# Kernel optimization log

Hardware: AMD Instinct MI355X
Metric: run time of the kernel (lower is better)

## Reference

```python
import jax, jax.numpy as jnp
import numpy as np

B, S, HID = 2, 2048, 4096
H, KV, D = 32, 8, 128
WINDOW = 512
ROPE_THETA = 10000.0


def _rope(x, positions):
    # x: [B, S, h, D]; neox rotate-half over full head_dim
    half = D // 2
    inv_freq = 1.0 / (ROPE_THETA ** (jnp.arange(0, half, dtype=jnp.float32) / half))
    ang = positions.astype(jnp.float32)[..., None] * inv_freq  # [B,S,half]
    cos = jnp.cos(ang)[:, :, None, :]
    sin = jnp.sin(ang)[:, :, None, :]
    x1, x2 = x[..., :half], x[..., half:]
    return jnp.concatenate([x1 * cos - x2 * sin, x2 * cos + x1 * sin], axis=-1)


def _smooth(x, filt):
    # x: [B, S, KV, D]; filt: [2, KV] -> out[t] = prev[t-1]*filt[0] + cur[t]*filt[1]
    prev = jnp.pad(x[:, :-1], ((0, 0), (1, 0), (0, 0), (0, 0)))  # zero at t=0
    return x * filt[1][None, None, :, None] + prev * filt[0][None, None, :, None]


def setup_inputs() -> dict:
    key = jax.random.key(0)
    k1, k2, k3, k4, k5 = jax.random.split(key, 5)
    return {
        "hidden_states": jax.random.normal(k1, (B, S, HID), jnp.float32) * 0.02,
        "positions": jnp.broadcast_to(jnp.arange(S, dtype=jnp.int32), (B, S)),
        "w_pack": jax.random.normal(k2, (HID, (H + 2 * KV) * D), jnp.float32) * (HID ** -0.5),
        "w_o": jax.random.normal(k3, (H * D, HID), jnp.float32) * ((H * D) ** -0.5),
        "conv_k": jax.random.normal(k4, (2, KV), jnp.float32) * 0.5,
        "conv_v": jax.random.normal(k5, (2, KV), jnp.float32) * 0.5,
    }


def reference(hidden_states, positions, w_pack, w_o, conv_k, conv_v):
    qkv = jnp.einsum("bsh,hf->bsf", hidden_states, w_pack)
    q = qkv[..., : H * D].reshape(B, S, H, D)
    k = qkv[..., H * D : (H + KV) * D].reshape(B, S, KV, D)
    v = qkv[..., (H + KV) * D :].reshape(B, S, KV, D)

    # causal depthwise smoothing of k/v (window 2), BEFORE rope
    k = _smooth(k, conv_k)
    v = _smooth(v, conv_v)

    q = _rope(q, positions)
    k = _rope(k, positions)

    g = H // KV  # GQA group size
    k_rep = jnp.repeat(k, g, axis=2)  # [B,S,H,D]
    v_rep = jnp.repeat(v, g, axis=2)

    scale = D ** -0.5
    scores = jnp.einsum("bqhd,bkhd->bhqk", q, k_rep) * scale
    qi = jnp.arange(S)[:, None]
    ki = jnp.arange(S)[None, :]
    mask = (ki <= qi) & (qi - ki < WINDOW)  # causal sliding window
    scores = jnp.where(mask[None, None], scores, jnp.float32(-1e30))
    probs = jax.nn.softmax(scores, axis=-1)
    attn = jnp.einsum("bhqk,bkhd->bqhd", probs, v_rep).reshape(B, S, H * D)
    return jnp.einsum("bsf,fh->bsh", attn, w_o)
```

## Files before the change

kernel.cpp:

```cpp
#include <hip/hip_runtime.h>
#include <stdint.h>

typedef unsigned short u16;
typedef unsigned int   u32;
typedef __bf16 bf16_t;
typedef __attribute__((ext_vector_type(8))) bf16_t bf16x8;
typedef __attribute__((ext_vector_type(4))) float   f32x4;

#define AS_GLOBAL __attribute__((address_space(1)))
#define AS_LDS    __attribute__((address_space(3)))

__device__ __forceinline__ void glds16(const u16* g, u16* l) {
  __builtin_amdgcn_global_load_lds((const AS_GLOBAL u32*)g, (AS_LDS u32*)l, 16, 0, 0);
}
__device__ __forceinline__ u16 f2bf(float f) {
  union { float f; u32 u; } a; a.f = f;
  return (u16)((a.u + 0x7FFFu + ((a.u >> 16) & 1u)) >> 16);
}
__device__ __forceinline__ float bf2f(u16 s) {
  union { u32 u; float f; } a; a.u = ((u32)s) << 16;
  return a.f;
}
union U16x8 { uint4 u; bf16x8 v; };

__global__ __launch_bounds__(256) void cvt_bf16(const float* __restrict__ X, u16* __restrict__ Y) {
  int i = blockIdx.x * 256 + threadIdx.x;
  float4 v = ((const float4*)X)[i];
  ushort4 o; o.x = f2bf(v.x); o.y = f2bf(v.y); o.z = f2bf(v.z); o.w = f2bf(v.w);
  ((ushort4*)Y)[i] = o;
}

__global__ __launch_bounds__(256) void cvt_transpose(const float* __restrict__ W, u16* __restrict__ Wt,
                                                     int K, int N) {
  __shared__ float t[64][65];
  const int n0 = blockIdx.x * 64, k0 = blockIdx.y * 64;
  const int tid = threadIdx.x;
  const int cr = tid >> 4, cc = (tid & 15) * 4;
#pragma unroll
  for (int p = 0; p < 4; ++p) {
    int r = p * 16 + cr;
    float4 v = *(const float4*)&W[(size_t)(k0 + r) * N + n0 + cc];
    t[r][cc] = v.x; t[r][cc + 1] = v.y; t[r][cc + 2] = v.z; t[r][cc + 3] = v.w;
  }
  __syncthreads();
#pragma unroll
  for (int p = 0; p < 4; ++p) {
    int rr = p * 16 + cr;
    ushort4 o;
    o.x = f2bf(t[cc + 0][rr]); o.y = f2bf(t[cc + 1][rr]);
    o.z = f2bf(t[cc + 2][rr]); o.w = f2bf(t[cc + 3][rr]);
    *(ushort4*)&Wt[(size_t)(n0 + rr) * K + k0 + cc] = o;
  }
}

template <int WRITE_BF16>
__global__ __launch_bounds__(256) void gemm_bt(const u16* __restrict__ A, const u16* __restrict__ Bt,
                                               void* __restrict__ C, int N, int K) {
  __shared__ u16 lA[128 * 32];
  __shared__ u16 lB[128 * 32];
  const int tid = threadIdx.x;
  const int w = tid >> 6, l = tid & 63;
  const int col = l & 15, quad = l >> 4;
  const int m0 = blockIdx.y * 128, n0 = blockIdx.x * 128;
  const int wm = (w >> 1) * 64, wn = (w & 1) * 64;

  f32x4 acc[4][4];
#pragma unroll
  for (int i = 0; i < 4; ++i)
#pragma unroll
    for (int j = 0; j < 4; ++j) acc[i][j] = f32x4{0.f, 0.f, 0.f, 0.f};

  const int srow = l >> 2, scol = (l & 3) * 8;
  const u16* Ab = A + (size_t)m0 * K;
  const u16* Bb = Bt + (size_t)n0 * K;

  for (int k0 = 0; k0 < K; k0 += 32) {
    __syncthreads();
#pragma unroll
    for (int i = 0; i < 2; ++i) {
      int chunk = w * 2 + i;
      int row = chunk * 16 + srow;
      glds16(Ab + (size_t)row * K + k0 + scol, &lA[chunk * 512]);
      glds16(Bb + (size_t)row * K + k0 + scol, &lB[chunk * 512]);
    }
    __syncthreads();
    bf16x8 af[4], bfr[4];
#pragma unroll
    for (int t = 0; t < 4; ++t) {
      af[t]  = *(const bf16x8*)&lA[(wm + t * 16 + col) * 32 + quad * 8];
      bfr[t] = *(const bf16x8*)&lB[(wn + t * 16 + col) * 32 + quad * 8];
    }
#pragma unroll
    for (int i = 0; i < 4; ++i)
#pragma unroll
      for (int j = 0; j < 4; ++j)
        acc[i][j] = __builtin_amdgcn_mfma_f32_16x16x32_bf16(af[i], bfr[j], acc[i][j], 0, 0, 0);
  }
  if (WRITE_BF16) {
    u16* Cb = (u16*)C;
#pragma unroll
    for (int i = 0; i < 4; ++i)
#pragma unroll
      for (int r = 0; r < 4; ++r) {
        int m = m0 + wm + i * 16 + quad * 4 + r;
        u16* rp = Cb + (size_t)m * N + n0 + wn + col;
#pragma unroll
        for (int j = 0; j < 4; ++j) rp[j * 16] = f2bf(acc[i][j][r]);
      }
  } else {
    float* Cf = (float*)C;
#pragma unroll
    for (int i = 0; i < 4; ++i)
#pragma unroll
      for (int r = 0; r < 4; ++r) {
        int m = m0 + wm + i * 16 + quad * 4 + r;
        float* rp = Cf + (size_t)m * N + n0 + wn + col;
#pragma unroll
        for (int j = 0; j < 4; ++j) rp[j * 16] = acc[i][j][r];
      }
  }
}

__global__ __launch_bounds__(256) void smooth_rope(const u16* __restrict__ QKV, const int* __restrict__ pos,
                                                   const float* __restrict__ ck, const float* __restrict__ cv,
                                                   u16* __restrict__ Q, u16* __restrict__ Kk, u16* __restrict__ V) {
  const int s = blockIdx.x, b = blockIdx.y, tid = threadIdx.x;
  const size_t base = (size_t)(b * 2048 + s) * 6144;
  const bool hasPrev = (s > 0);
  const size_t prev = base - 6144;
  const float p = (float)pos[b * 2048 + s];
  const float L2F = 0.20762050593046f;

  for (int e = tid; e < 2048; e += 256) {
    int h = e >> 6, i = e & 63;
    float x1 = bf2f(QKV[base + h * 128 + i]);
    float x2 = bf2f(QKV[base + h * 128 + 64 + i]);
    float ang = p * exp2f(-(float)i * L2F);
    float sn, cs; __sincosf(ang, &sn, &cs);
    size_t o = ((size_t)(b * 32 + h) * 2048 + s) * 128 + i;
    Q[o] = f2bf(x1 * cs - x2 * sn);
    Q[o + 64] = f2bf(x2 * cs + x1 * sn);
  }
  for (int e = tid; e < 512; e += 256) {
    int kv = e >> 6, i = e & 63;
    size_t off = 4096 + (size_t)kv * 128;
    float f0 = ck[kv], f1 = ck[8 + kv];
    float x1 = bf2f(QKV[base + off + i]) * f1;
    float x2 = bf2f(QKV[base + off + 64 + i]) * f1;
    if (hasPrev) {
      x1 += bf2f(QKV[prev + off + i]) * f0;
      x2 += bf2f(QKV[prev + off + 64 + i]) * f0;
    }
    float ang = p * exp2f(-(float)i * L2F);
    float sn, cs; __sincosf(ang, &sn, &cs);
    size_t o = ((size_t)(b * 8 + kv) * 2048 + s) * 128 + i;
    Kk[o] = f2bf(x1 * cs - x2 * sn);
    Kk[o + 64] = f2bf(x2 * cs + x1 * sn);
  }
  for (int e = tid; e < 1024; e += 256) {
    int kv = e >> 7, d = e & 127;
    size_t off = 5120 + (size_t)kv * 128 + d;
    float f0 = cv[kv], f1 = cv[8 + kv];
    float x = bf2f(QKV[base + off]) * f1;
    if (hasPrev) x += bf2f(QKV[prev + off]) * f0;
    V[((size_t)(b * 8 + kv) * 2048 + s) * 128 + d] = f2bf(x);
  }
}

__global__ __launch_bounds__(256) void transpose_v(const u16* __restrict__ V, u16* __restrict__ Vt) {
  __shared__ u16 t[64][72];
  const int s0 = blockIdx.x * 64, d0 = blockIdx.y * 64, bkv = blockIdx.z;
  const u16* src = V + (size_t)bkv * 2048 * 128;
  u16* dst = Vt + (size_t)bkv * 128 * 2048;
  const int tid = threadIdx.x;
  for (int e = tid; e < 4096; e += 256) {
    int r = e >> 6, c = e & 63;
    t[r][c] = src[(size_t)(s0 + r) * 128 + d0 + c];
  }
  __syncthreads();
  for (int e = tid; e < 4096; e += 256) {
    int r = e >> 6, c = e & 63;
    dst[(size_t)(d0 + r) * 2048 + s0 + c] = t[c][r];
  }
}

__global__ __launch_bounds__(256) void attn_fwd(const u16* __restrict__ Q, const u16* __restrict__ Kk,
                                                const u16* __restrict__ Vt, u16* __restrict__ O) {
  __shared__ union {
    struct { u16 k[64 * 136]; u16 v[128 * 72]; u16 p[4][16 * 72]; } s;
    u16 epi[64 * 136];
  } sm;
  const int tid = threadIdx.x, w = tid >> 6, l = tid & 63;
  const int col = l & 15, quad = l >> 4;
  const int q0 = blockIdx.x * 64;
  const int bh = blockIdx.y;
  const int b = bh >> 5, h = bh & 31, kv = h >> 2;
  const int qrow = q0 + w * 16 + col;
  const int qlo = q0 + w * 16;

  bf16x8 qf[4];
  {
    const u16* qp = Q + ((size_t)((b * 32 + h) * 2048 + qrow)) * 128 + quad * 8;
#pragma unroll
    for (int dc = 0; dc < 4; ++dc) { U16x8 u; u.u = *(const uint4*)(qp + dc * 32); qf[dc] = u.v; }
  }
  const u16* Kbase = Kk + (size_t)(b * 8 + kv) * 2048 * 128;
  const u16* Vbase = Vt + (size_t)(b * 8 + kv) * 128 * 2048;

  f32x4 of[8];
#pragma unroll
  for (int i = 0; i < 8; ++i) of[i] = f32x4{0.f, 0.f, 0.f, 0.f};
  float m_i = -3.0e38f, l_i = 0.f;

  const int s_lo = q0 >= 511 ? q0 - 511 : 0;
  const int kt_lo = s_lo >> 6, kt_hi = q0 >> 6;

  for (int kt = kt_lo; kt <= kt_hi; ++kt) {
    const int k0 = kt * 64;
    __syncthreads();
    for (int sg = tid; sg < 1024; sg += 256) {
      int kr = sg >> 4, kc = sg & 15;
      uint4 kd = *(const uint4*)(Kbase + (size_t)(k0 + kr) * 128 + kc * 8);
      *(uint4*)&sm.s.k[kr * 136 + kc * 8] = kd;
      int vr = sg >> 3, vc = sg & 7;
      uint4 vd = *(const uint4*)(Vbase + (size_t)vr * 2048 + k0 + vc * 8);
      *(uint4*)&sm.s.v[vr * 72 + vc * 8] = vd;
    }
    __syncthreads();

    f32x4 st[4];
#pragma unroll
    for (int t = 0; t < 4; ++t) {
      st[t] = f32x4{0.f, 0.f, 0.f, 0.f};
#pragma unroll
      for (int dc = 0; dc < 4; ++dc) {
        bf16x8 a = *(const bf16x8*)&sm.s.k[(t * 16 + col) * 136 + dc * 32 + quad * 8];
        st[t] = __builtin_amdgcn_mfma_f32_16x16x32_bf16(a, qf[dc], st[t], 0, 0, 0);
      }
    }
    const bool full = (k0 + 63 <= qlo) && (qlo + 15 - k0 < 512);
    float pmax = -3.0e38f;
#pragma unroll
    for (int t = 0; t < 4; ++t)
#pragma unroll
      for (int r = 0; r < 4; ++r) {
        float v = st[t][r] * 0.08838834764831845f;
        if (!full) {
          int key = k0 + t * 16 + quad * 4 + r;
          if (key > qrow || qrow - key >= 512) v = -1.0e30f;
        }
        st[t][r] = v;
        pmax = fmaxf(pmax, v);
      }
    pmax = fmaxf(pmax, __shfl_xor(pmax, 16, 64));
    pmax = fmaxf(pmax, __shfl_xor(pmax, 32, 64));
    float m_new = fmaxf(m_i, pmax);
    float alpha = __expf(m_i - m_new);
    float rsum = 0.f;
#pragma unroll
    for (int t = 0; t < 4; ++t) {
      u16 pk[4];
#pragma unroll
      for (int r = 0; r < 4; ++r) {
        float e = __expf(st[t][r] - m_new);
        rsum += e;
        pk[r] = f2bf(e);
      }
      u32 lo = (u32)pk[0] | ((u32)pk[1] << 16);
      u32 hi = (u32)pk[2] | ((u32)pk[3] << 16);
      *(uint2*)&sm.s.p[w][col * 72 + t * 16 + quad * 4] = make_uint2(lo, hi);
    }
    rsum += __shfl_xor(rsum, 16, 64);
    rsum += __shfl_xor(rsum, 32, 64);
    l_i = l_i * alpha + rsum;
    m_i = m_new;
#pragma unroll
    for (int i = 0; i < 8; ++i) {
      of[i][0] *= alpha; of[i][1] *= alpha; of[i][2] *= alpha; of[i][3] *= alpha;
    }
#pragma unroll
    for (int c = 0; c < 2; ++c) {
      bf16x8 pb = *(const bf16x8*)&sm.s.p[w][col * 72 + c * 32 + quad * 8];
#pragma unroll
      for (int dt = 0; dt < 8; ++dt) {
        bf16x8 a = *(const bf16x8*)&sm.s.v[(dt * 16 + col) * 72 + c * 32 + quad * 8];
        of[dt] = __builtin_amdgcn_mfma_f32_16x16x32_bf16(a, pb, of[dt], 0, 0, 0);
      }
    }
  }
  float invl = 1.f / l_i;
  __syncthreads();
#pragma unroll
  for (int dt = 0; dt < 8; ++dt) {
    u16 pk[4];
#pragma unroll
    for (int r = 0; r < 4; ++r) pk[r] = f2bf(of[dt][r] * invl);
    u32 lo = (u32)pk[0] | ((u32)pk[1] << 16);
    u32 hi = (u32)pk[2] | ((u32)pk[3] << 16);
    *(uint2*)&sm.epi[(w * 16 + col) * 136 + dt * 16 + quad * 4] = make_uint2(lo, hi);
  }
  __syncthreads();
  for (int e = tid; e < 1024; e += 256) {
    int r = e >> 4, c = e & 15;
    uint4 v = *(const uint4*)&sm.epi[r * 136 + c * 8];
    *(uint4*)(O + ((size_t)(b * 2048 + q0 + r) * 4096 + h * 128 + c * 8)) = v;
  }
}

extern "C" void kernel_launch(void* const* d_in, const int* in_sizes, int n_in,
                              void* d_out, int out_size, void* d_ws, size_t ws_size,
                              hipStream_t stream) {
  const float* hs  = (const float*)d_in[0];
  const int*   pos = (const int*)d_in[1];
  const float* wp  = (const float*)d_in[2];
  const float* wo  = (const float*)d_in[3];
  const float* ck  = (const float*)d_in[4];
  const float* cv  = (const float*)d_in[5];
  float* out = (float*)d_out;
  char* ws = (char*)d_ws;

  u16* Xb   = (u16*)(ws);
  u16* Wt   = (u16*)(ws + 33554432);
  u16* QKV  = (u16*)(ws + 83886080);
  u16* Qb   = (u16*)(ws + 134217728);
  u16* Kb   = (u16*)(ws + 167772160);
  u16* Vb   = (u16*)(ws + 176160768);
  u16* Vtb  = (u16*)(ws + 184549376);
  u16* Attn = Xb;
  u16* Wot  = Wt;

  cvt_bf16<<<16384, 256, 0, stream>>>(hs, Xb);
  cvt_transpose<<<dim3(96, 64), 256, 0, stream>>>(wp, Wt, 4096, 6144);
  gemm_bt<1><<<dim3(48, 32), 256, 0, stream>>>(Xb, Wt, (void*)QKV, 6144, 4096);
  smooth_rope<<<dim3(2048, 2), 256, 0, stream>>>(QKV, pos, ck, cv, Qb, Kb, Vb);
  transpose_v<<<dim3(32, 2, 16), 256, 0, stream>>>(Vb, Vtb);
  attn_fwd<<<dim3(32, 64), 256, 0, stream>>>(Qb, Kb, Vtb, Attn);
  cvt_transpose<<<dim3(64, 64), 256, 0, stream>>>(wo, Wot, 4096, 4096);
  gemm_bt<0><<<dim3(32, 32), 256, 0, stream>>>(Attn, Wot, (void*)out, 4096, 4096);
}
```

Baseline: 808.8 us.

## Replace GEMM with 512-thread double-buffered swizzled 256xBN tile kernel

Replaces the simple 128x128 single-buffered GEMM with a 512-thread kernel that computes 256xBN tiles (BN=192 for QKV, 256 for the output projection). It double-buffers LDS with a K-step of 64 and issues the next stage's global-to-LDS loads in between the MFMA phases, using explicit vmcnt waits and raw barriers. LDS rows use an XOR swizzle to avoid bank conflicts, and s_setprio raises priority around the MFMA bursts. The aim is to hide memory latency and raise MFMA utilisation in the two big GEMMs. In exchange the kernel uses many more registers and more LDS per block, and the hand-tuned waitcnt counts are fragile.

```diff
diff --git a/kernel.cpp b/kernel.cpp
--- a/kernel.cpp
+++ b/kernel.cpp
@@ -53,70 +53,148 @@
   }
 }
 
-template <int WRITE_BF16>
-__global__ __launch_bounds__(256) void gemm_bt(const u16* __restrict__ A, const u16* __restrict__ Bt,
-                                               void* __restrict__ C, int N, int K) {
-  __shared__ u16 lA[128 * 32];
-  __shared__ u16 lB[128 * 32];
+__device__ __forceinline__ void stage256(const u16* gb, u16* ldst, int K, int kc, int tid, int w) {
+#pragma unroll
+  for (int s = 0; s < 2; ++s) {
+    int t = s * 512 + tid;
+    int row = t >> 2;
+    int slot = (t & 3) ^ ((row >> 1) & 3);
+    glds16(gb + (size_t)row * K + kc + slot * 8, ldst + s * 4096 + w * 512);
+  }
+}
+template <int BN>
+__device__ __forceinline__ void stageB(const u16* gb, u16* ldst, int K, int k0, int tid, int w) {
+  constexpr int NB = BN / 64;
+#pragma unroll
+  for (int s = 0; s < NB; ++s) {
+    int t = s * 512 + tid;
+    int rr = t >> 2;
+    int kh = rr >= BN ? 1 : 0;
+    int row = rr - kh * BN;
+    int slot = (t & 3) ^ ((row >> 1) & 3);
+    glds16(gb + (size_t)row * K + k0 + kh * 32 + slot * 8, ldst + s * 4096 + w * 512);
+  }
+}
+
+template <int BN, int WRITE_BF16>
+__global__ __launch_bounds__(512, 2) void gemm8p(const u16* __restrict__ A, const u16* __restrict__ Bt,
+                                                 void* __restrict__ C, int N, int K) {
+  constexpr int NF = BN / 64;
+  constexpr int NB = BN / 64;
+  constexpr int A_U16 = 2 * 256 * 32;
+  constexpr int B_U16 = 2 * BN * 32;
+  constexpr int BUF = A_U16 + B_U16;
+  __shared__ __align__(16) u16 lds[2 * BUF];
+
   const int tid = threadIdx.x;
   const int w = tid >> 6, l = tid & 63;
   const int col = l & 15, quad = l >> 4;
-  const int m0 = blockIdx.y * 128, n0 = blockIdx.x * 128;
-  const int wm = (w >> 1) * 64, wn = (w & 1) * 64;
-
-  f32x4 acc[4][4];
-#pragma unroll
-  for (int i = 0; i < 4; ++i)
-#pragma unroll
-    for (int j = 0; j < 4; ++j) acc[i][j] = f32x4{0.f, 0.f, 0.f, 0.f};
-
-  const int srow = l >> 2, scol = (l & 3) * 8;
+  const int m0 = blockIdx.y * 256, n0 = blockIdx.x * BN;
+  const int wm = (w >> 2) * 128;
+  const int wn = (w & 3) * (BN / 4);
+
+  f32x4 acc[8][NF];
+#pragma unroll
+  for (int i = 0; i < 8; ++i)
+#pragma unroll
+    for (int j = 0; j < NF; ++j) acc[i][j] = f32x4{0.f, 0.f, 0.f, 0.f};
+
+  const int sx = ((quad ^ ((col >> 1) & 3)) << 3);
+  const int aoff = (wm + col) * 32 + sx;
+  const int boff = (wn + col) * 32 + sx;
+
   const u16* Ab = A + (size_t)m0 * K;
   const u16* Bb = Bt + (size_t)n0 * K;
-
-  for (int k0 = 0; k0 < K; k0 += 32) {
-    __syncthreads();
-#pragma unroll
-    for (int i = 0; i < 2; ++i) {
-      int chunk = w * 2 + i;
-      int row = chunk * 16 + srow;
-      glds16(Ab + (size_t)row * K + k0 + scol, &lA[chunk * 512]);
-      glds16(Bb + (size_t)row * K + k0 + scol, &lB[chunk * 512]);
-    }
-    __syncthreads();
-    bf16x8 af[4], bfr[4];
-#pragma unroll
-    for (int t = 0; t < 4; ++t) {
-      af[t]  = *(const bf16x8*)&lA[(wm + t * 16 + col) * 32 + quad * 8];
-      bfr[t] = *(const bf16x8*)&lB[(wn + t * 16 + col) * 32 + quad * 8];
-    }
-#pragma unroll
-    for (int i = 0; i < 4; ++i)
-#pragma unroll
-      for (int j = 0; j < 4; ++j)
-        acc[i][j] = __builtin_amdgcn_mfma_f32_16x16x32_bf16(af[i], bfr[j], acc[i][j], 0, 0, 0);
-  }
+  const int NT = K >> 6;
+
+  stage256(Ab, &lds[0], K, 0, tid, w);
+  stageB<BN>(Bb, &lds[A_U16], K, 0, tid, w);
+  stage256(Ab, &lds[8192], K, 32, tid, w);
+
+  for (int t = 0; t < NT; ++t) {
+    const int c = t & 1;
+    const u16* lA = &lds[c * BUF];
+    const u16* lB = &lds[c * BUF + A_U16];
+    u16* nA = &lds[(c ^ 1) * BUF];
+    u16* nB = &lds[(c ^ 1) * BUF + A_U16];
+    const int kn = (t + 1) << 6;
+    const bool last = (t == NT - 1);
+
+    bf16x8 a[8], b[NF];
+    asm volatile("s_waitcnt vmcnt(2)" ::: "memory");
+    __builtin_amdgcn_s_barrier();
+    __builtin_amdgcn_sched_barrier(0);
+#pragma unroll
+    for (int i = 0; i < 8; ++i) a[i] = *(const bf16x8*)&lA[i * 512 + aoff];
+    b[0] = *(const bf16x8*)&lB[boff];
+    b[1] = *(const bf16x8*)&lB[512 + boff];
+    if (!last) stage256(Ab, nA, K, kn, tid, w);
+    __builtin_amdgcn_s_setprio(1);
+#pragma unroll
+    for (int i = 0; i < 8; ++i) {
+      acc[i][0] = __builtin_amdgcn_mfma_f32_16x16x32_bf16(a[i], b[0], acc[i][0], 0, 0, 0);
+      acc[i][1] = __builtin_amdgcn_mfma_f32_16x16x32_bf16(a[i], b[1], acc[i][1], 0, 0, 0);
+    }
+    __builtin_amdgcn_s_setprio(0);
+#pragma unroll
+    for (int j = 2; j < NF; ++j) b[j] = *(const bf16x8*)&lB[j * 512 + boff];
+    if (!last) stageB<BN>(Bb, nB, K, kn, tid, w);
+    __builtin_amdgcn_s_setprio(1);
+#pragma unroll
+    for (int i = 0; i < 8; ++i)
+#pragma unroll
+      for (int j = 2; j < NF; ++j)
+        acc[i][j] = __builtin_amdgcn_mfma_f32_16x16x32_bf16(a[i], b[j], acc[i][j], 0, 0, 0);
+    __builtin_amdgcn_s_setprio(0);
+    if (last) { asm volatile("s_waitcnt vmcnt(0)" ::: "memory"); }
+    else if (BN == 256) { asm volatile("s_waitcnt vmcnt(6)" ::: "memory"); }
+    else { asm volatile("s_waitcnt vmcnt(5)" ::: "memory"); }
+    __builtin_amdgcn_s_barrier();
+    __builtin_amdgcn_sched_barrier(0);
+#pragma unroll
+    for (int i = 0; i < 8; ++i) a[i] = *(const bf16x8*)&lA[8192 + i * 512 + aoff];
+    b[0] = *(const bf16x8*)&lB[B_U16 / 2 + boff];
+    b[1] = *(const bf16x8*)&lB[B_U16 / 2 + 512 + boff];
+    if (!last) stage256(Ab, nA + 8192, K, kn + 32, tid, w);
+    __builtin_amdgcn_s_setprio(1);
+#pragma unroll
+    for (int i = 0; i < 8; ++i) {
+      acc[i][0] = __builtin_amdgcn_mfma_f32_16x16x32_bf16(a[i], b[0], acc[i][0], 0, 0, 0);
+      acc[i][1] = __builtin_amdgcn_mfma_f32_16x16x32_bf16(a[i], b[1], acc[i][1], 0, 0, 0);
+    }
+    __builtin_amdgcn_s_setprio(0);
+#pragma unroll
+    for (int j = 2; j < NF; ++j) b[j] = *(const bf16x8*)&lB[B_U16 / 2 + j * 512 + boff];
+    __builtin_amdgcn_s_setprio(1);
+#pragma unroll
+    for (int i = 0; i < 8; ++i)
+#pragma unroll
+      for (int j = 2; j < NF; ++j)
+        acc[i][j] = __builtin_amdgcn_mfma_f32_16x16x32_bf16(a[i], b[j], acc[i][j], 0, 0, 0);
+    __builtin_amdgcn_s_setprio(0);
+  }
+
   if (WRITE_BF16) {
     u16* Cb = (u16*)C;
 #pragma unroll
-    for (int i = 0; i < 4; ++i)
+    for (int i = 0; i < 8; ++i)
 #pragma unroll
       for (int r = 0; r < 4; ++r) {
         int m = m0 + wm + i * 16 + quad * 4 + r;
         u16* rp = Cb + (size_t)m * N + n0 + wn + col;
 #pragma unroll
-        for (int j = 0; j < 4; ++j) rp[j * 16] = f2bf(acc[i][j][r]);
+        for (int j = 0; j < NF; ++j) rp[j * 16] = f2bf(acc[i][j][r]);
       }
   } else {
     float* Cf = (float*)C;
 #pragma unroll
-    for (int i = 0; i < 4; ++i)
+    for (int i = 0; i < 8; ++i)
 #pragma unroll
       for (int r = 0; r < 4; ++r) {
         int m = m0 + wm + i * 16 + quad * 4 + r;
         float* rp = Cf + (size_t)m * N + n0 + wn + col;
 #pragma unroll
-        for (int j = 0; j < 4; ++j) rp[j * 16] = acc[i][j][r];
+        for (int j = 0; j < NF; ++j) rp[j * 16] = acc[i][j][r];
       }
   }
 }
@@ -331,10 +409,10 @@
 
   cvt_bf16<<<16384, 256, 0, stream>>>(hs, Xb);
   cvt_transpose<<<dim3(96, 64), 256, 0, stream>>>(wp, Wt, 4096, 6144);
-  gemm_bt<1><<<dim3(48, 32), 256, 0, stream>>>(Xb, Wt, (void*)QKV, 6144, 4096);
+  gemm8p<192, 1><<<dim3(32, 16), 512, 0, stream>>>(Xb, Wt, (void*)QKV, 6144, 4096);
   smooth_rope<<<dim3(2048, 2), 256, 0, stream>>>(QKV, pos, ck, cv, Qb, Kb, Vb);
   transpose_v<<<dim3(32, 2, 16), 256, 0, stream>>>(Vb, Vtb);
   attn_fwd<<<dim3(32, 64), 256, 0, stream>>>(Qb, Kb, Vtb, Attn);
   cvt_transpose<<<dim3(64, 64), 256, 0, stream>>>(wo, Wot, 4096, 4096);
-  gemm_bt<0><<<dim3(32, 32), 256, 0, stream>>>(Attn, Wot, (void*)out, 4096, 4096);
-}
+  gemm8p<256, 0><<<dim3(16, 16), 512, 0, stream>>>(Attn, Wot, (void*)out, 4096, 4096);
+}
```

New measurement: 649.4 us. 19.7% less time.
